# Performance work log

Hardware: AMD Instinct MI355X
Metric: run time of the kernel (lower is better)

## Reference

```python
import jax, jax.numpy as jnp
import numpy as np


def setup_inputs() -> dict:
    key = jax.random.key(0)
    kx, ky, kq, kk, kv = jax.random.split(key, 5)
    B, S, D = 4, 4096, 1024
    scale = 1.0 / np.sqrt(D)
    return {
        "X": jax.random.normal(kx, (B, S, D), dtype=jnp.float32),
        "Y": jax.random.normal(ky, (B, S, D), dtype=jnp.float32),
        "Wq": jax.random.normal(kq, (D, D), dtype=jnp.float32) * scale,
        "Wk": jax.random.normal(kk, (D, D), dtype=jnp.float32) * scale,
        "Wv": jax.random.normal(kv, (D, D), dtype=jnp.float32) * scale,
    }


def reference(X, Y, Wq, Wk, Wv):
    # Single-head windowed cross attention.
    # torch nn.Linear(y) == y @ W.T
    WINDOW = 256
    B, S, D = X.shape
    Q = jnp.einsum("bsd,ed->bse", Y, Wq)
    K = jnp.einsum("bsd,ed->bse", X, Wk)
    V = jnp.einsum("bsd,ed->bse", X, Wv)
    scores = jnp.einsum("bqd,bkd->bqk", Q, K) / jnp.sqrt(jnp.float32(D))
    i = jnp.arange(S)
    band = jnp.abs(i[:, None] - i[None, :]) <= WINDOW  # [S, S]
    NEG = jnp.float32(-1e10)  # matches torch masked_fill value
    scores = jnp.where(band[None, :, :], scores, NEG)
    attn = jax.nn.softmax(scores, axis=-1)
    return jnp.einsum("bqk,bkd->bqd", attn, V)
```

## Files before the change

kernel.cpp:

```cpp
#include <hip/hip_runtime.h>
#include <hip/hip_bf16.h>
#include <stdint.h>

typedef _Float16 half8 __attribute__((ext_vector_type(8)));
typedef float floatx4 __attribute__((ext_vector_type(4)));

#define MFMA16(a, b, c) __builtin_amdgcn_mfma_f32_16x16x32_f16(a, b, c, 0, 0, 0)

__device__ __forceinline__ void async_load16(const void* g, void* l) {
    __builtin_amdgcn_global_load_lds((__attribute__((address_space(1))) void*)(g),
                                     (__attribute__((address_space(3))) void*)(l),
                                     16, 0, 0);
}

#define RAW_BARRIER()  asm volatile("s_barrier" ::: "memory")
#define WAIT_VMCNT(n)  asm volatile("s_waitcnt vmcnt(" #n ")" ::: "memory")
#define WAIT_LGKM0()   asm volatile("s_waitcnt lgkmcnt(0)" ::: "memory")


__global__ __launch_bounds__(256) void cvt_kernel(const float* __restrict__ in,
                                                  _Float16* __restrict__ out,
                                                  int n, float scale) {
    int i = (blockIdx.x * 256 + threadIdx.x) * 8;
    if (i >= n) return;
    float4 v0 = *(const float4*)(in + i);
    float4 v1 = *(const float4*)(in + i + 4);
    half8 h;
    h[0] = (_Float16)(v0.x * scale);
    h[1] = (_Float16)(v0.y * scale);
    h[2] = (_Float16)(v0.z * scale);
    h[3] = (_Float16)(v0.w * scale);
    h[4] = (_Float16)(v1.x * scale);
    h[5] = (_Float16)(v1.y * scale);
    h[6] = (_Float16)(v1.z * scale);
    h[7] = (_Float16)(v1.w * scale);
    *(half8*)(out + i) = h;
}

__global__ __launch_bounds__(512, 2) void gemm_bt(const _Float16* __restrict__ A,
                                                  const _Float16* __restrict__ B,
                                                  _Float16* __restrict__ C,
                                                  int M, int N, int K) {
    __shared__ _Float16 sA[2][2][256 * 32];
    __shared__ _Float16 sB[2][2][256 * 32];
    const int tid  = threadIdx.x;
    const int lane = tid & 63;
    const int w    = tid >> 6;
    const int quad = lane >> 4;
    const int m16  = lane & 15;
    const int mq   = (w >> 2) * 64;
    const int nq   = (w & 3) * 32;

    const int gx = gridDim.x, gy = gridDim.y;
    const int total = gx * gy;
    const int id = blockIdx.y * gx + blockIdx.x;
    const int logical = (id & 7) * (total >> 3) + (id >> 3);
    int bx, by;
    if (gx <= gy) { bx = logical % gx; by = logical / gx; }
    else          { by = logical % gy; bx = logical / gy; }
    const long row0 = (long)by * 256;
    const long col0 = (long)bx * 256;

    floatx4 acc[8][4] = {};

    const int swz = ((tid & 3) ^ ((tid >> 3) & 3)) * 8;
    const _Float16* ga = A + (row0 + (tid >> 2)) * (long)K + swz;
    const _Float16* gb = B + (col0 + (tid >> 2)) * (long)K + swz;
    const int wchunk = w * 1024;

    auto stageA = [&](int tile, int half) {
        const int s = tile & 1;
        char* l0 = (char*)sA[s][0] + half * 8192 + wchunk;
        char* l1 = (char*)sA[s][1] + half * 8192 + wchunk;
        const _Float16* g = ga + (long)tile * 64 + (long)half * 128 * K;
        async_load16(g, l0);
        async_load16(g + 32, l1);
    };
    auto stageB = [&](int tile, int half) {
        const int s = tile & 1;
        char* l0 = (char*)sB[s][0] + half * 8192 + wchunk;
        char* l1 = (char*)sB[s][1] + half * 8192 + wchunk;
        const _Float16* g = gb + (long)tile * 64 + (long)half * 128 * K;
        async_load16(g, l0);
        async_load16(g + 32, l1);
    };

    const int rswz = (m16 >> 1) & 3;
    const int NTt  = K >> 6;

    stageA(0, 0); stageA(0, 1); stageB(0, 0); stageB(0, 1);
    stageA(1, 0); stageB(1, 0);
    WAIT_VMCNT(4);
    RAW_BARRIER();

    for (int U = 0; U < NTt; ++U) {
        const int s = U & 1;
        const int T1 = U + 1, T2 = U + 2;
        half8 af[4][2], bf[2][2];
#pragma unroll
        for (int p = 0; p < 4; ++p) {
            const int mh = p >> 1, nh = p & 1;
            if ((p & 1) == 0) {
#pragma unroll
                for (int mt = 0; mt < 4; mt++)
#pragma unroll
                    for (int j = 0; j < 2; j++)
                        af[mt][j] = *(const half8*)(sA[s][j] +
                            (mh * 128 + mq + mt * 16 + m16) * 32 + (quad ^ rswz) * 8);
            }
#pragma unroll
            for (int nt = 0; nt < 2; nt++)
#pragma unroll
                for (int j = 0; j < 2; j++)
                    bf[nt][j] = *(const half8*)(sB[s][j] +
                        (nh * 128 + nq + nt * 16 + m16) * 32 + (quad ^ rswz) * 8);
            if (p == 0 && T1 < NTt) stageB(T1, 1);
            if (p == 1 && T1 < NTt) stageA(T1, 1);
            if (p == 2 && T2 < NTt) stageA(T2, 0);
            if (p == 3 && T2 < NTt) stageB(T2, 0);
            if (p == 3) {
                if (T2 < NTt) { WAIT_VMCNT(4); }
                else          { WAIT_VMCNT(0); }
            }
            RAW_BARRIER();
            WAIT_LGKM0();
            __builtin_amdgcn_sched_barrier(0);
            __builtin_amdgcn_s_setprio(1);
#pragma unroll
            for (int mt = 0; mt < 4; mt++)
#pragma unroll
                for (int nt = 0; nt < 2; nt++) {
                    acc[mh * 4 + mt][nh * 2 + nt] =
                        MFMA16(af[mt][0], bf[nt][0], acc[mh * 4 + mt][nh * 2 + nt]);
                    acc[mh * 4 + mt][nh * 2 + nt] =
                        MFMA16(af[mt][1], bf[nt][1], acc[mh * 4 + mt][nh * 2 + nt]);
                }
            __builtin_amdgcn_s_setprio(0);
            RAW_BARRIER();
        }
    }

#pragma unroll
    for (int mt = 0; mt < 8; mt++)
#pragma unroll
        for (int nt = 0; nt < 4; nt++)
#pragma unroll
            for (int reg = 0; reg < 4; reg++) {
                long r = row0 + (mt >> 2) * 128 + mq + (mt & 3) * 16 + quad * 4 + reg;
                long c = col0 + (nt >> 1) * 128 + nq + (nt & 1) * 16 + m16;
                C[r * N + c] = (_Float16)acc[mt][nt][reg];
            }
}

__global__ __launch_bounds__(512) void qk_kernel(const _Float16* __restrict__ Qh,
                                                 const _Float16* __restrict__ Kh,
                                                 _Float16* __restrict__ Pg,
                                                 float* __restrict__ invSum) {
    const int S = 4096, D = 1024;
    __shared__ _Float16 sK[2][576 * 32];
    __shared__ _Float16 sQ[2][64 * 32];
    __shared__ float sMax[64][8];
    __shared__ float sSum[64][8];

    const int tid  = threadIdx.x;
    const int lane = tid & 63;
    const int w    = tid >> 6;
    const int quad = lane >> 4;
    const int c16  = lane & 15;
    const int qblk = (blockIdx.x & 7) * 32 + (blockIdx.x >> 3);
    const int b    = qblk >> 6;
    const int q0   = (qblk & 63) << 6;

    int kstart = q0 - 256; if (kstart < 0) kstart = 0;
    int kend   = q0 + 320; if (kend > S) kend = S;
    const int ntReal = (kend - kstart) >> 4;

    const int lrow = lane >> 2;
    const int swz  = ((lane & 3) ^ ((lane >> 3) & 3)) * 8;
    const _Float16* Kbase = Kh + ((long)(b * S + kstart) + lrow) * D + swz;
    const _Float16* Qbase = Qh + ((long)(b * S + q0) + w * 16 + lrow) * D + swz;

    auto stage = [&](int bi, int kc) {
#pragma unroll
        for (int j = 0; j < 5; j++) {
            if (j < 4 || w < 4) {
                int g = j * 8 + w;
                async_load16(Kbase + (long)g * 16 * D + kc, (char*)sK[bi] + g * 1024);
            }
        }
        if (w < 4)
            async_load16(Qbase + kc, (char*)sQ[bi] + w * 1024);
    };

    const int rswz = ((c16 >> 1) & 3);

    floatx4 acc[4][5] = {};
    stage(0, 0);
    stage(1, 32);
    for (int kc = 0; kc < 1024; kc += 32) {
        const int bi = (kc >> 5) & 1;
        if (kc + 32 < 1024) {
            if (w < 4) { WAIT_VMCNT(6); } else { WAIT_VMCNT(4); }
        } else {
            WAIT_VMCNT(0);
        }
        RAW_BARRIER();
        half8 aQ[4];
#pragma unroll
        for (int mt = 0; mt < 4; mt++)
            aQ[mt] = *(const half8*)(sQ[bi] + (mt * 16 + c16) * 32 + (quad ^ rswz) * 8);
#pragma unroll
        for (int i = 0; i < 5; i++) {
            if (i < 4 || w < 4) {
                int t = w + i * 8;
                half8 bK = *(const half8*)(sK[bi] + (t * 16 + c16) * 32 + (quad ^ rswz) * 8);
#pragma unroll
                for (int mt = 0; mt < 4; mt++)
                    acc[mt][i] = MFMA16(aQ[mt], bK, acc[mt][i]);
            }
        }
        WAIT_LGKM0();
        RAW_BARRIER();
        if (kc + 64 < 1024) stage(bi, kc + 64);
    }

#pragma unroll
    for (int i = 0; i < 5; i++) {
        if (i < 4 || w < 4) {
            int t = w + i * 8;
            int j = kstart + t * 16 + c16;
            bool pad = (t >= ntReal);
#pragma unroll
            for (int mt = 0; mt < 4; mt++)
#pragma unroll
                for (int r = 0; r < 4; r++) {
                    int qi = q0 + mt * 16 + quad * 4 + r;
                    int dd = qi - j; dd = dd < 0 ? -dd : dd;
                    if (dd > 256 || pad) acc[mt][i][r] = -1e30f;
                }
        }
    }
#pragma unroll
    for (int mt = 0; mt < 4; mt++)
#pragma unroll
        for (int r = 0; r < 4; r++) {
            float m = -1e30f;
#pragma unroll
            for (int i = 0; i < 5; i++)
                if (i < 4 || w < 4) m = fmaxf(m, acc[mt][i][r]);
#pragma unroll
            for (int off = 1; off < 16; off <<= 1) m = fmaxf(m, __shfl_xor(m, off, 64));
            if (c16 == 0) sMax[mt * 16 + quad * 4 + r][w] = m;
        }
    __syncthreads();
    if (tid < 64) {
        float fm = sMax[tid][0];
#pragma unroll
        for (int j = 1; j < 8; j++) fm = fmaxf(fm, sMax[tid][j]);
        sMax[tid][0] = fm;
    }
    __syncthreads();
#pragma unroll
    for (int mt = 0; mt < 4; mt++)
#pragma unroll
        for (int r = 0; r < 4; r++) {
            int row = mt * 16 + quad * 4 + r;
            float fm = sMax[row][0];
            float s = 0.f;
#pragma unroll
            for (int i = 0; i < 5; i++) {
                if (i < 4 || w < 4) {
                    int t = w + i * 8;
                    float e = __expf(acc[mt][i][r] - fm);
                    s += e;
                    if (t < ntReal)
                        Pg[(long)qblk * 36864 + row * 576 + t * 16 + c16] = (_Float16)e;
                }
            }
#pragma unroll
            for (int off = 1; off < 16; off <<= 1) s += __shfl_xor(s, off, 64);
            if (c16 == 0) sSum[row][w] = s;
        }
    __syncthreads();
    if (tid < 64) {
        float t = 0.f;
#pragma unroll
        for (int j = 0; j < 8; j++) t += sSum[tid][j];
        invSum[qblk * 64 + tid] = 1.f / t;
    }
}

__global__ __launch_bounds__(512) void pv_kernel(const _Float16* __restrict__ Pg,
                                                 const float* __restrict__ invSum,
                                                 const _Float16* __restrict__ Vt,
                                                 float* __restrict__ out) {
    const int S = 4096, D = 1024, TOK = 16384;
    __shared__ _Float16 sA[2][64 * 32];
    __shared__ _Float16 sB[2][256 * 32];

    const int tid  = threadIdx.x;
    const int lane = tid & 63;
    const int w    = tid >> 6;
    const int quad = lane >> 4;
    const int c16  = lane & 15;

    const int logical = (blockIdx.x & 7) * 128 + (blockIdx.x >> 3);
    const int qblk = logical >> 2;
    const int n0   = (logical & 3) << 8;
    const int b    = qblk >> 6;
    const int q0   = (qblk & 63) << 6;

    int kstart = q0 - 256; if (kstart < 0) kstart = 0;
    int kend   = q0 + 320; if (kend > S) kend = S;
    const int nsteps = (kend - kstart) >> 5;

    const int lrow = lane >> 2;
    const int swz  = ((lane & 3) ^ ((lane >> 3) & 3)) * 8;
    const _Float16* Abase = Pg + (long)qblk * 36864 + (w * 16 + lrow) * 576 + swz;
    const _Float16* Bbase = Vt + (long)(n0 + lrow) * TOK + b * S + kstart + swz;

    auto stage = [&](int bi, int kc) {
        if (w < 4)
            async_load16(Abase + kc, (char*)sA[bi] + w * 1024);
#pragma unroll
        for (int j = 0; j < 2; j++) {
            int g = j * 8 + w;
            async_load16(Bbase + (long)g * 16 * TOK + kc, (char*)sB[bi] + g * 1024);
        }
    };

    const int wm = (w >> 2) * 32;
    const int wn = (w & 3) * 64;
    const int rswz = ((c16 >> 1) & 3);
    floatx4 acc[2][4] = {};

    stage(0, 0);
    stage(1, 32);
    for (int s = 0; s < nsteps; s++) {
        const int bi = s & 1;
        if (s + 1 < nsteps) {
            if (w < 4) { WAIT_VMCNT(3); } else { WAIT_VMCNT(2); }
        } else {
            WAIT_VMCNT(0);
        }
        RAW_BARRIER();
        half8 aA[2], bB[4];
#pragma unroll
        for (int mt = 0; mt < 2; mt++)
            aA[mt] = *(const half8*)(sA[bi] + (wm + mt * 16 + c16) * 32 + (quad ^ rswz) * 8);
#pragma unroll
        for (int nt = 0; nt < 4; nt++)
            bB[nt] = *(const half8*)(sB[bi] + (wn + nt * 16 + c16) * 32 + (quad ^ rswz) * 8);
#pragma unroll
        for (int mt = 0; mt < 2; mt++)
#pragma unroll
            for (int nt = 0; nt < 4; nt++)
                acc[mt][nt] = MFMA16(aA[mt], bB[nt], acc[mt][nt]);
        WAIT_LGKM0();
        RAW_BARRIER();
        if (s + 2 < nsteps) stage(bi, (s + 2) * 32);
    }

    const float* isB = invSum + qblk * 64;
#pragma unroll
    for (int mt = 0; mt < 2; mt++)
#pragma unroll
        for (int nt = 0; nt < 4; nt++)
#pragma unroll
            for (int reg = 0; reg < 4; reg++) {
                int row = wm + mt * 16 + quad * 4 + reg;
                int col = n0 + wn + nt * 16 + c16;
                out[(long)(b * S + q0 + row) * D + col] = acc[mt][nt][reg] * isB[row];
            }
}

extern "C" void kernel_launch(void* const* d_in, const int* in_sizes, int n_in,
                              void* d_out, int out_size, void* d_ws, size_t ws_size,
                              hipStream_t stream) {
    const float* X  = (const float*)d_in[0];
    const float* Y  = (const float*)d_in[1];
    const float* Wq = (const float*)d_in[2];
    const float* Wk = (const float*)d_in[3];
    const float* Wv = (const float*)d_in[4];
    float* out = (float*)d_out;

    const long NTOK = 16384, D = 1024;
    char* p = (char*)d_ws;
    _Float16* Xh  = (_Float16*)p; p += NTOK * D * 2;
    _Float16* Yh  = (_Float16*)p; p += NTOK * D * 2;
    _Float16* Wqh = (_Float16*)p; p += D * D * 2;
    _Float16* Wkh = (_Float16*)p; p += D * D * 2;
    _Float16* Wvh = (_Float16*)p; p += D * D * 2;
    _Float16* Qh  = (_Float16*)p; p += NTOK * D * 2;
    _Float16* Vt  = (_Float16*)p; p += NTOK * D * 2;
    _Float16* Kh  = Yh;
    _Float16* Pg  = Xh;
    float* invSum = (float*)(Xh + 256l * 64 * 576);

    const int nT = (int)(NTOK * D);
    const int nW = (int)(D * D);
    cvt_kernel<<<nT / 2048, 256, 0, stream>>>(X, Xh, nT, 1.f);
    cvt_kernel<<<nT / 2048, 256, 0, stream>>>(Y, Yh, nT, 1.f);
    cvt_kernel<<<nW / 2048, 256, 0, stream>>>(Wq, Wqh, nW, 0.03125f);
    cvt_kernel<<<nW / 2048, 256, 0, stream>>>(Wk, Wkh, nW, 1.f);
    cvt_kernel<<<nW / 2048, 256, 0, stream>>>(Wv, Wvh, nW, 1.f);

    gemm_bt<<<dim3(1024 / 256, 16384 / 256), 512, 0, stream>>>(Yh, Wqh, Qh, 16384, 1024, 1024);
    gemm_bt<<<dim3(1024 / 256, 16384 / 256), 512, 0, stream>>>(Xh, Wkh, Kh, 16384, 1024, 1024);
    gemm_bt<<<dim3(16384 / 256, 1024 / 256), 512, 0, stream>>>(Wvh, Xh, Vt, 1024, 16384, 1024);

    qk_kernel<<<dim3(256), 512, 0, stream>>>(Qh, Kh, Pg, invSum);
    pv_kernel<<<dim3(4 * 256), 512, 0, stream>>>(Pg, invSum, Vt, out);
}
```

Baseline: 377.4 us.

## Triple-buffer QK kernel loads and merge conversion launches

The QK score kernel moves from double to triple buffering of K and Q tiles in shared memory. It prefetches three stages ahead with adjusted vmcnt waits so global loads have more time to overlap MFMA work. Separately, the five fp32-to-fp16 conversion launches are merged into two kernels (X/Y together, three weights together) to cut launch overhead. The extra LDS buffer raises shared memory use per block, which may limit occupancy.

```diff
diff --git a/kernel.cpp b/kernel.cpp
--- a/kernel.cpp
+++ b/kernel.cpp
@@ -18,22 +18,44 @@
 #define WAIT_LGKM0()   asm volatile("s_waitcnt lgkmcnt(0)" ::: "memory")
 
 
-__global__ __launch_bounds__(256) void cvt_kernel(const float* __restrict__ in,
-                                                  _Float16* __restrict__ out,
-                                                  int n, float scale) {
-    int i = (blockIdx.x * 256 + threadIdx.x) * 8;
-    if (i >= n) return;
+__global__ __launch_bounds__(256) void cvt2_kernel(const float* __restrict__ in0,
+                                                   _Float16* __restrict__ out0, int n0,
+                                                   const float* __restrict__ in1,
+                                                   _Float16* __restrict__ out1) {
+    long i = ((long)blockIdx.x * 256 + threadIdx.x) * 8;
+    const float* in; _Float16* out;
+    if (i < n0) { in = in0 + i; out = out0 + i; }
+    else        { in = in1 + (i - n0); out = out1 + (i - n0); }
+    float4 v0 = *(const float4*)(in);
+    float4 v1 = *(const float4*)(in + 4);
+    half8 h;
+    h[0] = (_Float16)v0.x; h[1] = (_Float16)v0.y;
+    h[2] = (_Float16)v0.z; h[3] = (_Float16)v0.w;
+    h[4] = (_Float16)v1.x; h[5] = (_Float16)v1.y;
+    h[6] = (_Float16)v1.z; h[7] = (_Float16)v1.w;
+    *(half8*)(out) = h;
+}
+
+__global__ __launch_bounds__(256) void cvt3w_kernel(const float* __restrict__ wq,
+                                                    const float* __restrict__ wk,
+                                                    const float* __restrict__ wv,
+                                                    _Float16* __restrict__ oq,
+                                                    _Float16* __restrict__ ok,
+                                                    _Float16* __restrict__ ov) {
+    const int nW8 = (1024 * 1024) / 8;
+    int idx = blockIdx.x * 256 + threadIdx.x;
+    int seg = idx / nW8;
+    long i = (long)(idx - seg * nW8) * 8;
+    const float* in = (seg == 0) ? wq : (seg == 1) ? wk : wv;
+    _Float16* out   = (seg == 0) ? oq : (seg == 1) ? ok : ov;
+    float scale = (seg == 0) ? 0.03125f : 1.f;
     float4 v0 = *(const float4*)(in + i);
     float4 v1 = *(const float4*)(in + i + 4);
     half8 h;
-    h[0] = (_Float16)(v0.x * scale);
-    h[1] = (_Float16)(v0.y * scale);
-    h[2] = (_Float16)(v0.z * scale);
-    h[3] = (_Float16)(v0.w * scale);
-    h[4] = (_Float16)(v1.x * scale);
-    h[5] = (_Float16)(v1.y * scale);
-    h[6] = (_Float16)(v1.z * scale);
-    h[7] = (_Float16)(v1.w * scale);
+    h[0] = (_Float16)(v0.x * scale); h[1] = (_Float16)(v0.y * scale);
+    h[2] = (_Float16)(v0.z * scale); h[3] = (_Float16)(v0.w * scale);
+    h[4] = (_Float16)(v1.x * scale); h[5] = (_Float16)(v1.y * scale);
+    h[6] = (_Float16)(v1.z * scale); h[7] = (_Float16)(v1.w * scale);
     *(half8*)(out + i) = h;
 }
 
@@ -157,8 +179,8 @@
                                                  _Float16* __restrict__ Pg,
                                                  float* __restrict__ invSum) {
     const int S = 4096, D = 1024;
-    __shared__ _Float16 sK[2][576 * 32];
-    __shared__ _Float16 sQ[2][64 * 32];
+    __shared__ _Float16 sK[3][576 * 32];
+    __shared__ _Float16 sQ[3][64 * 32];
     __shared__ float sMax[64][8];
     __shared__ float sSum[64][8];
 
@@ -197,9 +219,13 @@
     floatx4 acc[4][5] = {};
     stage(0, 0);
     stage(1, 32);
+    stage(2, 64);
     for (int kc = 0; kc < 1024; kc += 32) {
-        const int bi = (kc >> 5) & 1;
-        if (kc + 32 < 1024) {
+        const int st = kc >> 5;
+        const int bi = st % 3;
+        if (st <= 29) {
+            if (w < 4) { WAIT_VMCNT(12); } else { WAIT_VMCNT(8); }
+        } else if (st == 30) {
             if (w < 4) { WAIT_VMCNT(6); } else { WAIT_VMCNT(4); }
         } else {
             WAIT_VMCNT(0);
@@ -221,7 +247,7 @@
         }
         WAIT_LGKM0();
         RAW_BARRIER();
-        if (kc + 64 < 1024) stage(bi, kc + 64);
+        if (st + 3 <= 31) stage(bi, kc + 96);
     }
 
 #pragma unroll
@@ -398,12 +424,8 @@
     float* invSum = (float*)(Xh + 256l * 64 * 576);
 
     const int nT = (int)(NTOK * D);
-    const int nW = (int)(D * D);
-    cvt_kernel<<<nT / 2048, 256, 0, stream>>>(X, Xh, nT, 1.f);
-    cvt_kernel<<<nT / 2048, 256, 0, stream>>>(Y, Yh, nT, 1.f);
-    cvt_kernel<<<nW / 2048, 256, 0, stream>>>(Wq, Wqh, nW, 0.03125f);
-    cvt_kernel<<<nW / 2048, 256, 0, stream>>>(Wk, Wkh, nW, 1.f);
-    cvt_kernel<<<nW / 2048, 256, 0, stream>>>(Wv, Wvh, nW, 1.f);
+    cvt2_kernel<<<(2 * nT) / 2048, 256, 0, stream>>>(X, Xh, nT, Y, Yh);
+    cvt3w_kernel<<<(3 * 1024 * 1024) / 2048, 256, 0, stream>>>(Wq, Wk, Wv, Wqh, Wkh, Wvh);
 
     gemm_bt<<<dim3(1024 / 256, 16384 / 256), 512, 0, stream>>>(Yh, Wqh, Qh, 16384, 1024, 1024);
     gemm_bt<<<dim3(1024 / 256, 16384 / 256), 512, 0, stream>>>(Xh, Wkh, Kh, 16384, 1024, 1024);
```

After: 370.0 us. 1.02x faster.
